# Performance work log

Hardware: AMD Instinct MI355X
Metric: run time of the kernel (lower is better)

## Reference

```python
import jax, jax.numpy as jnp
import numpy as np

H = 32          # num_attention_heads
ROPE_BASE = 10000.0


def _rotary_freqs_cis(seq_len: int, head_dim: int) -> jnp.ndarray:
    # complex e^{i * pos * theta_j}, shape [seq_len, head_dim//2]
    inv_freq = 1.0 / (ROPE_BASE ** (jnp.arange(0, head_dim, 2, dtype=jnp.float32) / head_dim))
    angles = jnp.arange(seq_len, dtype=jnp.float32)[:, None] * inv_freq[None, :]
    return jax.lax.complex(jnp.cos(angles), jnp.sin(angles))


def _apply_rotary(u: jnp.ndarray, freqs_cis: jnp.ndarray) -> jnp.ndarray:
    # u: [B, S, H, hd]; faithful to apply_rotary_emb (interleaved pairs -> complex mul)
    ur = u.astype(jnp.float32).reshape(*u.shape[:-1], -1, 2)
    uc = jax.lax.complex(ur[..., 0], ur[..., 1])
    # freqs_cis broadcast: [1, S, 1, hd//2]
    uc = uc * freqs_cis[None, :, None, :]
    return jnp.stack((jnp.real(uc), jnp.imag(uc)), axis=-1).reshape(u.shape)


def setup_inputs() -> dict:
    key = jax.random.key(0)
    ks = jax.random.split(key, 5)
    B, S, D = 1, 2048, 4096
    init_std = 0.02
    x = jax.random.normal(ks[0], (B, S, D), dtype=jnp.float32)
    wq = jax.random.normal(ks[1], (D, D), dtype=jnp.float32) * init_std
    wk = jax.random.normal(ks[2], (D, D), dtype=jnp.float32) * init_std
    wv = jax.random.normal(ks[3], (D, D), dtype=jnp.float32) * init_std
    wo = jax.random.normal(ks[4], (D, D), dtype=jnp.float32) * init_std
    return {"x": x, "wq": wq, "wk": wk, "wv": wv, "wo": wo}


def reference(x, wq, wk, wv, wo):
    B, S, D = x.shape
    hd = D // H  # head_dim = 128
    q = (x @ wq).reshape(B, S, H, hd)
    k = (x @ wk).reshape(B, S, H, hd)
    v = (x @ wv).reshape(B, S, H, hd)

    freqs_cis = _rotary_freqs_cis(S, hd)
    q = _apply_rotary(q, freqs_cis)
    k = _apply_rotary(k, freqs_cis)
    # n_rep == 1 (num_key_value_heads == num_attention_heads) -> repeat_kv is identity

    scale = 1.0 / jnp.sqrt(jnp.float32(hd))
    scores = jnp.einsum('bqhd,bkhd->bhqk', q, k) * scale  # [B, H, S, S]
    causal = jnp.tril(jnp.ones((S, S), dtype=bool))
    neg = jnp.finfo(scores.dtype).min
    scores = jnp.where(causal[None, None, :, :], scores, neg)
    probs = jax.nn.softmax(scores, axis=-1)
    attn = jnp.einsum('bhqk,bkhd->bqhd', probs, v).reshape(B, S, D)
    return attn @ wo
```

## Files before the change

### kernel.cpp

```cpp
#include <hip/hip_runtime.h>
#include <stdint.h>

#define S_LEN 2048
#define DMODEL 4096
#define NHEAD 32
#define HDIM 128

typedef __attribute__((ext_vector_type(8))) short bf16x8;
typedef __attribute__((ext_vector_type(4))) float f32x4;

__device__ __forceinline__ unsigned short f2bf(float f) {
    union { float f; unsigned u; } v; v.f = f;
    unsigned u = v.u;
    unsigned r = (u + 0x7FFFu + ((u >> 16) & 1u)) >> 16;
    return (unsigned short)r;
}
__device__ __forceinline__ float bf2f(unsigned short h) {
    union { unsigned u; float f; } v; v.u = ((unsigned)h) << 16;
    return v.f;
}

__global__ void convert_x_kernel(const float* __restrict__ x,
                                 unsigned short* __restrict__ xb, int n4) {
    int t = blockIdx.x * blockDim.x + threadIdx.x;
    if (t >= n4) return;
    float4 v = ((const float4*)x)[t];
    ushort4 o;
    o.x = f2bf(v.x); o.y = f2bf(v.y); o.z = f2bf(v.z); o.w = f2bf(v.w);
    ((ushort4*)xb)[t] = o;
}

__global__ void convert_wt_kernel(const float* __restrict__ w,
                                  unsigned short* __restrict__ wt) {
    __shared__ unsigned short t[64][65];
    int n0 = blockIdx.x * 64, k0 = blockIdx.y * 64;
    for (int i = 0; i < 16; ++i) {
        int o = threadIdx.x + i * 256;
        int r = o >> 6, c = o & 63;
        t[r][c] = f2bf(w[(size_t)(k0 + r) * DMODEL + n0 + c]);
    }
    __syncthreads();
    for (int i = 0; i < 16; ++i) {
        int o = threadIdx.x + i * 256;
        int rr = o >> 6, kk = o & 63;
        wt[(size_t)(n0 + rr) * DMODEL + k0 + kk] = t[kk][rr];
    }
}

template<int STORE_MODE>
__global__ __launch_bounds__(256, 2)
void gemm_bt_kernel(const unsigned short* __restrict__ A,
                    const unsigned short* __restrict__ BT,
                    void* __restrict__ C, int M, int N, int K) {
    __shared__ __align__(16) unsigned short As[128 * 32];
    __shared__ __align__(16) unsigned short Bs[128 * 32];
    const int lane = threadIdx.x & 63;
    const int w = threadIdx.x >> 6;
    const int wm = w & 1, wn = w >> 1;
    const int m0 = blockIdx.y * 128, n0 = blockIdx.x * 128;

    f32x4 zero = {0.f, 0.f, 0.f, 0.f};
    f32x4 acc[4][4];
    for (int i = 0; i < 4; ++i)
        for (int j = 0; j < 4; ++j) acc[i][j] = zero;

    const int lr = lane >> 2;
    const int lc = lane & 3;
    const int q = lane >> 4, lm = lane & 15;

    for (int k0 = 0; k0 < K; k0 += 32) {
        __syncthreads();
        for (int i = 0; i < 2; ++i) {
            int rb = w * 32 + i * 16;
            int r = rb + lr;
            int gc = lc ^ ((r >> 1) & 3);
            const unsigned short* ga = A + (size_t)(m0 + r) * K + k0 + gc * 8;
            __builtin_amdgcn_global_load_lds(
                (__attribute__((address_space(1))) unsigned int*)ga,
                (__attribute__((address_space(3))) unsigned int*)(&As[rb * 32]), 16, 0, 0);
            const unsigned short* gb = BT + (size_t)(n0 + r) * K + k0 + gc * 8;
            __builtin_amdgcn_global_load_lds(
                (__attribute__((address_space(1))) unsigned int*)gb,
                (__attribute__((address_space(3))) unsigned int*)(&Bs[rb * 32]), 16, 0, 0);
        }
        __syncthreads();
        bf16x8 af[4], bf[4];
        for (int t = 0; t < 4; ++t) {
            int ra = wm * 64 + t * 16 + lm;
            af[t] = *(const bf16x8*)&As[ra * 32 + ((q ^ ((ra >> 1) & 3)) * 8)];
            int rb2 = wn * 64 + t * 16 + lm;
            bf[t] = *(const bf16x8*)&Bs[rb2 * 32 + ((q ^ ((rb2 >> 1) & 3)) * 8)];
        }
        for (int mi = 0; mi < 4; ++mi)
            for (int ni = 0; ni < 4; ++ni)
                acc[mi][ni] = __builtin_amdgcn_mfma_f32_16x16x32_bf16(
                    af[mi], bf[ni], acc[mi][ni], 0, 0, 0);
    }

    for (int mi = 0; mi < 4; ++mi) {
        int mbase = m0 + wm * 64 + mi * 16 + q * 4;
        for (int ni = 0; ni < 4; ++ni) {
            int n = n0 + wn * 64 + ni * 16 + lm;
            if (STORE_MODE == 0) {
                unsigned short* Cb = (unsigned short*)C;
                for (int r = 0; r < 4; ++r)
                    Cb[(size_t)(mbase + r) * N + n] = f2bf(acc[mi][ni][r]);
            } else if (STORE_MODE == 1) {
                unsigned short* Cb = (unsigned short*)C;
                ushort4 v;
                v.x = f2bf(acc[mi][ni][0]); v.y = f2bf(acc[mi][ni][1]);
                v.z = f2bf(acc[mi][ni][2]); v.w = f2bf(acc[mi][ni][3]);
                *(ushort4*)&Cb[(size_t)n * M + mbase] = v;
            } else {
                float* Cf = (float*)C;
                for (int r = 0; r < 4; ++r)
                    Cf[(size_t)(mbase + r) * N + n] = acc[mi][ni][r];
            }
        }
    }
}

__global__ void rope_kernel(unsigned short* __restrict__ qb,
                            unsigned short* __restrict__ kb) {
    int t = blockIdx.x * blockDim.x + threadIdx.x;
    if (t >= S_LEN * DMODEL / 2) return;
    int s = t >> 11;
    int p = t & 2047;
    int j = p & 63;
    float ang = (float)s * exp2f((float)j * -0.2076205059304602f);
    float sn, cs;
    sincosf(ang, &sn, &cs);
    size_t idx = (size_t)s * DMODEL + 2 * p;
    const float SC = 0.08838834764831845f;
    float a0 = bf2f(qb[idx]), a1 = bf2f(qb[idx + 1]);
    qb[idx]     = f2bf((a0 * cs - a1 * sn) * SC);
    qb[idx + 1] = f2bf((a0 * sn + a1 * cs) * SC);
    float b0 = bf2f(kb[idx]), b1 = bf2f(kb[idx + 1]);
    kb[idx]     = f2bf(b0 * cs - b1 * sn);
    kb[idx + 1] = f2bf(b0 * sn + b1 * cs);
}

__global__ __launch_bounds__(256, 2)
void attn_kernel(const unsigned short* __restrict__ qb,
                 const unsigned short* __restrict__ kb,
                 const unsigned short* __restrict__ vt,
                 unsigned short* __restrict__ ab) {
    __shared__ __align__(16) unsigned short Ks[32 * 128];
    __shared__ __align__(16) unsigned short VTs[128 * 32];
    __shared__ __align__(16) unsigned short Pb[4][16 * 40];
    const int lane = threadIdx.x & 63;
    const int w = threadIdx.x >> 6;
    const int h = blockIdx.y;
    const int q0 = blockIdx.x * 64;
    const int qw = q0 + w * 16;
    const int q = lane >> 4, lm = lane & 15;

    bf16x8 qf[4];
    for (int kc = 0; kc < 4; ++kc)
        qf[kc] = *(const bf16x8*)&qb[(size_t)(qw + lm) * DMODEL + h * HDIM + kc * 32 + q * 8];

    f32x4 zero = {0.f, 0.f, 0.f, 0.f};
    f32x4 o[8];
    for (int i = 0; i < 8; ++i) o[i] = zero;
    float mrow[4] = {-1e30f, -1e30f, -1e30f, -1e30f};
    float lrow[4] = {0.f, 0.f, 0.f, 0.f};

    const int nch = q0 / 32 + 2;
    for (int c = 0; c < nch; ++c) {
        const int j0 = c * 32;
        __syncthreads();
        for (int i = 0; i < 2; ++i) {
            int rb = w * 8 + i * 4;
            int r = rb + (lane >> 4);
            int gc = (lane & 15) ^ (r & 15);
            const unsigned short* g = kb + (size_t)(j0 + r) * DMODEL + h * HDIM + gc * 8;
            __builtin_amdgcn_global_load_lds(
                (__attribute__((address_space(1))) unsigned int*)g,
                (__attribute__((address_space(3))) unsigned int*)(&Ks[rb * 128]), 16, 0, 0);
        }
        for (int i = 0; i < 2; ++i) {
            int db = w * 32 + i * 16;
            int d = db + (lane >> 2);
            int gc = (lane & 3) ^ ((d >> 1) & 3);
            const unsigned short* g = vt + (size_t)(h * HDIM + d) * S_LEN + j0 + gc * 8;
            __builtin_amdgcn_global_load_lds(
                (__attribute__((address_space(1))) unsigned int*)g,
                (__attribute__((address_space(3))) unsigned int*)(&VTs[db * 32]), 16, 0, 0);
        }
        __syncthreads();
        if (j0 > qw + 15) continue;

        f32x4 s0 = zero, s1 = zero;
        for (int kc = 0; kc < 4; ++kc) {
            bf16x8 kf0 = *(const bf16x8*)&Ks[lm * 128 + (((kc * 4 + q) ^ lm) * 8)];
            int kk1 = 16 + lm;
            bf16x8 kf1 = *(const bf16x8*)&Ks[kk1 * 128 + (((kc * 4 + q) ^ lm) * 8)];
            s0 = __builtin_amdgcn_mfma_f32_16x16x32_bf16(qf[kc], kf0, s0, 0, 0, 0);
            s1 = __builtin_amdgcn_mfma_f32_16x16x32_bf16(qf[kc], kf1, s1, 0, 0, 0);
        }
        if (j0 + 31 > qw) {
            for (int r = 0; r < 4; ++r) {
                int qq = qw + q * 4 + r;
                if (j0 + lm > qq)      s0[r] = -1e30f;
                if (j0 + 16 + lm > qq) s1[r] = -1e30f;
            }
        }
        float al[4], p0[4], p1[4];
        for (int r = 0; r < 4; ++r) {
            float mx = fmaxf(s0[r], s1[r]);
            mx = fmaxf(mx, __shfl_xor(mx, 1));
            mx = fmaxf(mx, __shfl_xor(mx, 2));
            mx = fmaxf(mx, __shfl_xor(mx, 4));
            mx = fmaxf(mx, __shfl_xor(mx, 8));
            float mn = fmaxf(mrow[r], mx);
            al[r] = __expf(mrow[r] - mn);
            mrow[r] = mn;
            p0[r] = __expf(s0[r] - mn);
            p1[r] = __expf(s1[r] - mn);
            float rs = p0[r] + p1[r];
            rs += __shfl_xor(rs, 1);
            rs += __shfl_xor(rs, 2);
            rs += __shfl_xor(rs, 4);
            rs += __shfl_xor(rs, 8);
            lrow[r] = lrow[r] * al[r] + rs;
        }
        for (int r = 0; r < 4; ++r) {
            Pb[w][(q * 4 + r) * 40 + lm]      = f2bf(p0[r]);
            Pb[w][(q * 4 + r) * 40 + 16 + lm] = f2bf(p1[r]);
        }
        bf16x8 pA = *(const bf16x8*)&Pb[w][lm * 40 + q * 8];
        for (int nt = 0; nt < 8; ++nt) {
            int d = lm + nt * 16;
            bf16x8 vf = *(const bf16x8*)&VTs[d * 32 + ((q ^ ((d >> 1) & 3)) * 8)];
            f32x4 oo = o[nt];
            for (int r = 0; r < 4; ++r) oo[r] *= al[r];
            o[nt] = __builtin_amdgcn_mfma_f32_16x16x32_bf16(pA, vf, oo, 0, 0, 0);
        }
    }
    float inv[4];
    for (int r = 0; r < 4; ++r) inv[r] = 1.0f / lrow[r];
    for (int nt = 0; nt < 8; ++nt) {
        int d = h * HDIM + lm + nt * 16;
        for (int r = 0; r < 4; ++r)
            ab[(size_t)(qw + q * 4 + r) * DMODEL + d] = f2bf(o[nt][r] * inv[r]);
    }
}

extern "C" void kernel_launch(void* const* d_in, const int* in_sizes, int n_in,
                              void* d_out, int out_size, void* d_ws, size_t ws_size,
                              hipStream_t stream) {
    const float* x  = (const float*)d_in[0];
    const float* wq = (const float*)d_in[1];
    const float* wk = (const float*)d_in[2];
    const float* wv = (const float*)d_in[3];
    const float* wo = (const float*)d_in[4];
    char* ws = (char*)d_ws;
    const size_t MB = 1024 * 1024;
    unsigned short* xb  = (unsigned short*)(ws + 0 * MB);
    unsigned short* qb  = (unsigned short*)(ws + 16 * MB);
    unsigned short* kb  = (unsigned short*)(ws + 32 * MB);
    unsigned short* vtb = (unsigned short*)(ws + 48 * MB);
    unsigned short* ab  = (unsigned short*)(ws + 64 * MB);
    unsigned short* wtb = (unsigned short*)(ws + 80 * MB);

    dim3 cg(64, 64);
    dim3 gg(32, 16);

    convert_x_kernel<<<(S_LEN * DMODEL / 4) / 256, 256, 0, stream>>>(x, xb, S_LEN * DMODEL / 4);

    convert_wt_kernel<<<cg, 256, 0, stream>>>(wq, wtb);
    gemm_bt_kernel<0><<<gg, 256, 0, stream>>>(xb, wtb, qb, S_LEN, DMODEL, DMODEL);
    convert_wt_kernel<<<cg, 256, 0, stream>>>(wk, wtb);
    gemm_bt_kernel<0><<<gg, 256, 0, stream>>>(xb, wtb, kb, S_LEN, DMODEL, DMODEL);
    convert_wt_kernel<<<cg, 256, 0, stream>>>(wv, wtb);
    gemm_bt_kernel<1><<<gg, 256, 0, stream>>>(xb, wtb, vtb, S_LEN, DMODEL, DMODEL);

    rope_kernel<<<(S_LEN * DMODEL / 2) / 256, 256, 0, stream>>>(qb, kb);

    attn_kernel<<<dim3(S_LEN / 64, NHEAD), 256, 0, stream>>>(qb, kb, vtb, ab);

    convert_wt_kernel<<<cg, 256, 0, stream>>>(wo, wtb);
    gemm_bt_kernel<2><<<gg, 256, 0, stream>>>(ab, wtb, d_out, S_LEN, DMODEL, DMODEL);
}
```

Baseline: 815.6 us.

## Use 64-key attention tiles with register prefetch and reversed block order

The attention kernel now processes 64-key chunks instead of 32. The next K/V tile is prefetched into registers while the current tile is computed, then written to LDS with an XOR swizzle. Blocks are issued in reverse so the longest causal query blocks start first, which should balance the tail. The aim is to hide global load latency and halve the number of barrier rounds, at the cost of more registers and LDS that may lower occupancy under launch_bounds(256,2).

```diff
diff --git a/kernel.cpp b/kernel.cpp
--- a/kernel.cpp
+++ b/kernel.cpp
@@ -145,15 +145,24 @@
                  const unsigned short* __restrict__ kb,
                  const unsigned short* __restrict__ vt,
                  unsigned short* __restrict__ ab) {
-    __shared__ __align__(16) unsigned short Ks[32 * 128];
-    __shared__ __align__(16) unsigned short VTs[128 * 32];
-    __shared__ __align__(16) unsigned short Pb[4][16 * 40];
-    const int lane = threadIdx.x & 63;
-    const int w = threadIdx.x >> 6;
+    __shared__ __align__(16) unsigned short Ks[64 * 128];
+    __shared__ __align__(16) unsigned short VTs[128 * 64];
+    __shared__ __align__(16) unsigned short Pb[4][16 * 72];
+    const int t = threadIdx.x;
+    const int lane = t & 63;
+    const int w = t >> 6;
     const int h = blockIdx.y;
-    const int q0 = blockIdx.x * 64;
+    const int q0 = ((int)gridDim.x - 1 - (int)blockIdx.x) * 64;
     const int qw = q0 + w * 16;
     const int q = lane >> 4, lm = lane & 15;
+
+    const int krow = t >> 2;
+    const int kcol = t & 3;
+    const int vrow = t >> 1;
+    const int vcol = t & 1;
+
+    const unsigned short* gK = kb + (size_t)krow * DMODEL + h * HDIM;
+    const unsigned short* gV = vt + (size_t)(h * HDIM + vrow) * S_LEN;
 
     bf16x8 qf[4];
     for (int kc = 0; kc < 4; ++kc)
@@ -165,49 +174,44 @@
     float mrow[4] = {-1e30f, -1e30f, -1e30f, -1e30f};
     float lrow[4] = {0.f, 0.f, 0.f, 0.f};
 
-    const int nch = q0 / 32 + 2;
+    const int nch = q0 / 64 + 1;
+
+    bf16x8 kreg[4], vreg[4];
+    for (int i = 0; i < 4; ++i) {
+        kreg[i] = *(const bf16x8*)&gK[(size_t)0 * DMODEL + (kcol + i * 4) * 8];
+        vreg[i] = *(const bf16x8*)&gV[0 + (vcol + i * 2) * 8];
+    }
+    for (int i = 0; i < 4; ++i) {
+        *(bf16x8*)&Ks[krow * 128 + (((kcol + i * 4) ^ (krow & 15)) * 8)] = kreg[i];
+        *(bf16x8*)&VTs[vrow * 64 + (((vcol + i * 2) ^ (vrow & 7)) * 8)] = vreg[i];
+    }
+    __syncthreads();
+
     for (int c = 0; c < nch; ++c) {
-        const int j0 = c * 32;
-        __syncthreads();
-        for (int i = 0; i < 2; ++i) {
-            int rb = w * 8 + i * 4;
-            int r = rb + (lane >> 4);
-            int gc = (lane & 15) ^ (r & 15);
-            const unsigned short* g = kb + (size_t)(j0 + r) * DMODEL + h * HDIM + gc * 8;
-            __builtin_amdgcn_global_load_lds(
-                (__attribute__((address_space(1))) unsigned int*)g,
-                (__attribute__((address_space(3))) unsigned int*)(&Ks[rb * 128]), 16, 0, 0);
-        }
-        for (int i = 0; i < 2; ++i) {
-            int db = w * 32 + i * 16;
-            int d = db + (lane >> 2);
-            int gc = (lane & 3) ^ ((d >> 1) & 3);
-            const unsigned short* g = vt + (size_t)(h * HDIM + d) * S_LEN + j0 + gc * 8;
-            __builtin_amdgcn_global_load_lds(
-                (__attribute__((address_space(1))) unsigned int*)g,
-                (__attribute__((address_space(3))) unsigned int*)(&VTs[db * 32]), 16, 0, 0);
-        }
-        __syncthreads();
-        if (j0 > qw + 15) continue;
-
-        f32x4 s0 = zero, s1 = zero;
-        for (int kc = 0; kc < 4; ++kc) {
-            bf16x8 kf0 = *(const bf16x8*)&Ks[lm * 128 + (((kc * 4 + q) ^ lm) * 8)];
-            int kk1 = 16 + lm;
-            bf16x8 kf1 = *(const bf16x8*)&Ks[kk1 * 128 + (((kc * 4 + q) ^ lm) * 8)];
-            s0 = __builtin_amdgcn_mfma_f32_16x16x32_bf16(qf[kc], kf0, s0, 0, 0, 0);
-            s1 = __builtin_amdgcn_mfma_f32_16x16x32_bf16(qf[kc], kf1, s1, 0, 0, 0);
-        }
-        if (j0 + 31 > qw) {
-            for (int r = 0; r < 4; ++r) {
-                int qq = qw + q * 4 + r;
-                if (j0 + lm > qq)      s0[r] = -1e30f;
-                if (j0 + 16 + lm > qq) s1[r] = -1e30f;
-            }
-        }
-        float al[4], p0[4], p1[4];
+        const int j0 = c * 64;
+        if (c + 1 < nch) {
+            const size_t jn = (size_t)(j0 + 64);
+            for (int i = 0; i < 4; ++i) {
+                kreg[i] = *(const bf16x8*)&gK[jn * DMODEL + (kcol + i * 4) * 8];
+                vreg[i] = *(const bf16x8*)&gV[jn + (vcol + i * 2) * 8];
+            }
+        }
+
+        f32x4 s[4];
+        for (int ks = 0; ks < 4; ++ks) s[ks] = zero;
+        for (int kc = 0; kc < 4; ++kc)
+            for (int ks = 0; ks < 4; ++ks) {
+                bf16x8 kf = *(const bf16x8*)&Ks[(ks * 16 + lm) * 128 + (((kc * 4 + q) ^ lm) * 8)];
+                s[ks] = __builtin_amdgcn_mfma_f32_16x16x32_bf16(qf[kc], kf, s[ks], 0, 0, 0);
+            }
+        if (c == nch - 1) {
+            for (int ks = 0; ks < 4; ++ks)
+                for (int r = 0; r < 4; ++r)
+                    if (j0 + ks * 16 + lm > qw + q * 4 + r) s[ks][r] = -1e30f;
+        }
+        float al[4];
         for (int r = 0; r < 4; ++r) {
-            float mx = fmaxf(s0[r], s1[r]);
+            float mx = fmaxf(fmaxf(s[0][r], s[1][r]), fmaxf(s[2][r], s[3][r]));
             mx = fmaxf(mx, __shfl_xor(mx, 1));
             mx = fmaxf(mx, __shfl_xor(mx, 2));
             mx = fmaxf(mx, __shfl_xor(mx, 4));
@@ -215,28 +219,42 @@
             float mn = fmaxf(mrow[r], mx);
             al[r] = __expf(mrow[r] - mn);
             mrow[r] = mn;
-            p0[r] = __expf(s0[r] - mn);
-            p1[r] = __expf(s1[r] - mn);
-            float rs = p0[r] + p1[r];
+            float rs = 0.f;
+            float pv[4];
+            for (int ks = 0; ks < 4; ++ks) {
+                pv[ks] = __expf(s[ks][r] - mn);
+                rs += pv[ks];
+            }
             rs += __shfl_xor(rs, 1);
             rs += __shfl_xor(rs, 2);
             rs += __shfl_xor(rs, 4);
             rs += __shfl_xor(rs, 8);
             lrow[r] = lrow[r] * al[r] + rs;
-        }
-        for (int r = 0; r < 4; ++r) {
-            Pb[w][(q * 4 + r) * 40 + lm]      = f2bf(p0[r]);
-            Pb[w][(q * 4 + r) * 40 + 16 + lm] = f2bf(p1[r]);
-        }
-        bf16x8 pA = *(const bf16x8*)&Pb[w][lm * 40 + q * 8];
+            for (int ks = 0; ks < 4; ++ks)
+                Pb[w][(q * 4 + r) * 72 + ks * 16 + lm] = f2bf(pv[ks]);
+        }
+        bf16x8 pA0 = *(const bf16x8*)&Pb[w][lm * 72 + q * 8];
+        bf16x8 pA1 = *(const bf16x8*)&Pb[w][lm * 72 + 32 + q * 8];
         for (int nt = 0; nt < 8; ++nt) {
-            int d = lm + nt * 16;
-            bf16x8 vf = *(const bf16x8*)&VTs[d * 32 + ((q ^ ((d >> 1) & 3)) * 8)];
+            int d = nt * 16 + lm;
+            bf16x8 vf0 = *(const bf16x8*)&VTs[d * 64 + ((q ^ (d & 7)) * 8)];
+            bf16x8 vf1 = *(const bf16x8*)&VTs[d * 64 + (((4 + q) ^ (d & 7)) * 8)];
             f32x4 oo = o[nt];
             for (int r = 0; r < 4; ++r) oo[r] *= al[r];
-            o[nt] = __builtin_amdgcn_mfma_f32_16x16x32_bf16(pA, vf, oo, 0, 0, 0);
-        }
-    }
+            oo = __builtin_amdgcn_mfma_f32_16x16x32_bf16(pA0, vf0, oo, 0, 0, 0);
+            o[nt] = __builtin_amdgcn_mfma_f32_16x16x32_bf16(pA1, vf1, oo, 0, 0, 0);
+        }
+
+        __syncthreads();
+        if (c + 1 < nch) {
+            for (int i = 0; i < 4; ++i) {
+                *(bf16x8*)&Ks[krow * 128 + (((kcol + i * 4) ^ (krow & 15)) * 8)] = kreg[i];
+                *(bf16x8*)&VTs[vrow * 64 + (((vcol + i * 2) ^ (vrow & 7)) * 8)] = vreg[i];
+            }
+        }
+        __syncthreads();
+    }
+
     float inv[4];
     for (int r = 0; r < 4; ++r) inv[r] = 1.0f / lrow[r];
     for (int nt = 0; nt < 8; ++nt) {
```

Result: no change. 801.9 us (-1.7%).
